# Optimization experiments

Hardware: AMD Instinct MI355X
Metric: run time of the kernel (lower is better)

Reference implementation:

```python
import jax, jax.numpy as jnp
import numpy as np

B, C, N, D, K, M, E, G = 2, 64, 16384, 3, 128, 1, 262144, 3


def setup_inputs() -> dict:
    key = jax.random.key(0)
    ks = jax.random.split(key, 15)
    scale = 1.0 / (C * C)
    return {
        "x": jax.random.normal(ks[0], (B, C, N), jnp.float32),
        "nodes": jax.random.uniform(ks[1], (B, N, D), jnp.float32),
        "node_weights": jax.random.uniform(ks[2], (B, N, M), jnp.float32),
        "geo": jax.random.normal(ks[3], (B, G, N), jnp.float32),
        "directed_edges": jax.random.randint(ks[4], (B, E, 2), 0, N, jnp.int32),
        "edge_gradient_weights": 0.1 * jax.random.normal(ks[5], (B, E, D), jnp.float32),
        "modes": jax.random.normal(ks[6], (K, D, M), jnp.float32),
        "weights_c": scale * jax.random.uniform(ks[7], (C, C, K, M), jnp.float32),
        "weights_s": scale * jax.random.uniform(ks[8], (C, C, K, M), jnp.float32),
        "weights_0": scale * jax.random.uniform(ks[9], (C, C, 1, M), jnp.float32),
        "W": jax.random.normal(ks[10], (C, C), jnp.float32) / np.sqrt(C),
        "gw": jax.random.normal(ks[11], (C, C * D), jnp.float32) / np.sqrt(C * D),
        "geo_wx": jax.random.normal(ks[12], (C, G), jnp.float32) / np.sqrt(G),
        "wx": jax.random.normal(ks[13], (C, C), jnp.float32) / np.sqrt(C),
        "w2": jax.random.normal(ks[14], (C, C), jnp.float32) / np.sqrt(C),
    }


def reference(x, nodes, node_weights, geo, directed_edges, edge_gradient_weights,
              modes, weights_c, weights_s, weights_0, W, gw, geo_wx, wx, w2):
    # ---- Fourier bases: cos(kx), sin(kx), 1 -------------------------------
    temp = jnp.einsum('bxd,kdw->bxkw', nodes, modes)          # [B,N,K,M]
    bases_c, bases_s = jnp.cos(temp), jnp.sin(temp)
    b, n = temp.shape[0], temp.shape[1]
    bases_0 = jnp.ones((b, n, 1, temp.shape[3]), temp.dtype)
    nw = node_weights[:, :, None, :]                          # quadrature weights
    wb_c, wb_s, wb_0 = bases_c * nw, bases_s * nw, bases_0 * nw

    # ---- Spectral convolution (non-uniform Fourier neural layer) ----------
    x_c = jnp.einsum('bix,bxkw->bikw', x, wb_c)
    x_s = -jnp.einsum('bix,bxkw->bikw', x, wb_s)
    x_0 = jnp.einsum('bix,bxkw->bikw', x, wb_0)
    f_c = jnp.einsum('bikw,iokw->bokw', x_c, weights_c) - jnp.einsum('bikw,iokw->bokw', x_s, weights_s)
    f_s = jnp.einsum('bikw,iokw->bokw', x_s, weights_c) + jnp.einsum('bikw,iokw->bokw', x_c, weights_s)
    f_0 = jnp.einsum('bikw,iokw->bokw', x_0, weights_0)
    x1 = (jnp.einsum('bokw,bxkw->box', f_0, bases_0)
          + 2.0 * jnp.einsum('bokw,bxkw->box', f_c, bases_c)
          - 2.0 * jnp.einsum('bokw,bxkw->box', f_s, bases_s))

    # ---- Pointwise linear W ----------------------------------------------
    x2 = jnp.einsum('oi,bix->box', W, x)

    # ---- Least-squares gradient via edge gather + scatter-add -------------
    fT = jnp.transpose(x, (0, 2, 1))                          # [B,N,C]
    tgt, src = directed_edges[..., 0], directed_edges[..., 1]  # [B,E]
    f_src = jnp.take_along_axis(fT, src[:, :, None], axis=1)   # [B,E,C]
    f_tgt = jnp.take_along_axis(fT, tgt[:, :, None], axis=1)
    df = f_src - f_tgt
    # message[b,e,c,d] = w[b,e,d] * df[b,e,c], flattened c-major -> [B,E,C*D]
    msg = (df[..., :, None] * edge_gradient_weights[..., None, :]).reshape(b, tgt.shape[1], -1)
    gradf = jnp.zeros((b, n, msg.shape[-1]), msg.dtype).at[jnp.arange(b)[:, None], tgt].add(msg)
    x3 = jnp.einsum('og,bng->bon', gw, gradf)                  # [B,C,N]

    # ---- Geo embedding: w2 @ (softsign(geo_wx@geo) * (wx@x)) --------------
    h = jax.nn.soft_sign(jnp.einsum('og,bgx->box', geo_wx, geo)) * jnp.einsum('oi,bix->box', wx, x)
    x4 = jnp.einsum('oi,bix->box', w2, h)

    return jax.nn.gelu(x1 + x2 + x3 + x4, approximate=False)
```

## Files before the change

kernel.cpp:

```cpp
#include <hip/hip_runtime.h>
#include <hip/hip_fp16.h>
#include <math.h>

#define BB 2
#define CC 64
#define NN 16384
#define DD 3
#define KK 128
#define EE 262144
#define GG 3
#define PP 128
#define LL (NN/PP)
#define KTOT 576

typedef short bf16x8 __attribute__((ext_vector_type(8)));
typedef float f32x4  __attribute__((ext_vector_type(4)));

__device__ __forceinline__ short f2bf(float f) {
    unsigned u = __float_as_uint(f);
    u += 0x7FFF + ((u >> 16) & 1);
    return (short)(u >> 16);
}
__device__ __forceinline__ float bf2f(unsigned short u) {
    return __uint_as_float(((unsigned)u) << 16);
}

constexpr size_t OFF_XB   = 0;
constexpr size_t OFF_PC   = OFF_XB   + (size_t)BB*NN*32;
constexpr size_t OFF_PS   = OFF_PC   + (size_t)BB*PP*CC*KK;
constexpr size_t OFF_BIN4 = OFF_PC;
constexpr size_t OFF_AC   = OFF_PS   + (size_t)BB*PP*CC*KK;
constexpr size_t OFF_AS   = OFF_AC   + (size_t)BB*CC*KK;
constexpr size_t OFF_F0   = OFF_AS   + (size_t)BB*CC*KK;
constexpr size_t OFF_X0   = OFF_F0   + (size_t)BB*CC;
constexpr size_t OFF_CNT  = OFF_X0   + (size_t)BB*CC;
constexpr size_t OFF_OFFS = OFF_CNT  + (size_t)BB*NN;
constexpr size_t OFF_RANK = OFF_OFFS + (size_t)BB*NN;
constexpr size_t OFF_GRB  = OFF_RANK + (size_t)BB*EE;
constexpr size_t OFF_APAN = OFF_GRB  + (size_t)BB*NN*96;
constexpr size_t OFF_GWXT = OFF_APAN + (size_t)BB*KTOT*CC/2;

__global__ void __launch_bounds__(256) k_pre(const float* __restrict__ x,
                                             const float* __restrict__ nwt,
                                             const int* __restrict__ edges,
                                             const float* __restrict__ W,
                                             const float* __restrict__ gw,
                                             const float* __restrict__ geo_wx,
                                             const float* __restrict__ w2,
                                             unsigned short* __restrict__ xB,
                                             float* __restrict__ x0,
                                             int* __restrict__ counts,
                                             int* __restrict__ rank,
                                             float* __restrict__ gwxT,
                                             short* __restrict__ ApanB) {
    int blk = blockIdx.x;
    int tid = threadIdx.x;
    __shared__ float tile[64][65];
    __shared__ float red[256];
    if (blk < BB*(NN/64)) {
        int b = blk / (NN/64);
        int n0 = (blk % (NN/64)) * 64;
        int c = tid & 63, r4 = tid >> 6;
        for (int rr = 0; rr < 16; rr++) {
            int i = r4*16 + rr;
            tile[i][c] = x[((size_t)b*CC + i)*NN + n0 + c];
        }
        __syncthreads();
        for (int rr = 0; rr < 16; rr++) {
            int nn = r4*16 + rr;
            xB[((size_t)b*NN + n0 + nn)*64 + c] = (unsigned short)f2bf(tile[c][nn]);
        }
    } else if (blk < BB*(NN/64) + BB*CC) {
        int bi = blk - BB*(NN/64);
        int b = bi >> 6, i = bi & 63;
        const float4* __restrict__ xr = (const float4*)&x[((size_t)b*CC + i)*NN];
        const float4* __restrict__ wr = (const float4*)&nwt[(size_t)b*NN];
        float s = 0.f;
        for (int t = tid; t < NN/4; t += 256) {
            float4 xv = xr[t];
            float4 wv = wr[t];
            s += xv.x*wv.x + xv.y*wv.y + xv.z*wv.z + xv.w*wv.w;
        }
        red[tid] = s;
        __syncthreads();
        for (int off = 128; off > 0; off >>= 1) {
            if (tid < off) red[tid] += red[tid+off];
            __syncthreads();
        }
        if (tid == 0) x0[b*CC + i] = red[0];
    } else if (blk < BB*(NN/64) + BB*CC + (BB*EE)/256) {
        int idx = (blk - (BB*(NN/64) + BB*CC))*256 + tid;
        if (idx < BB*EE) {
            int tgt = edges[(size_t)idx*2 + 0];
            int b = idx / EE;
            rank[idx] = atomicAdd(&counts[b*NN + tgt], 1);
        }
    } else {
        int idx = (blk - (BB*(NN/64) + BB*CC + (BB*EE)/256))*256 + tid;
        if (idx < CC*CC) {
            int j = idx>>6, o = idx&63;
            short wv  = f2bf(W[o*CC+j]);
            short w2v = f2bf(w2[o*CC+j]);
            ApanB[((size_t)(0*CC+o))*KTOT + 256 + j] = wv;
            ApanB[((size_t)(1*CC+o))*KTOT + 256 + j] = wv;
            ApanB[((size_t)(0*CC+o))*KTOT + 320 + j] = w2v;
            ApanB[((size_t)(1*CC+o))*KTOT + 320 + j] = w2v;
        }
        if (idx < CC*CC*DD) {
            int g = idx>>6, o = idx&63;
            short gv = f2bf(gw[o*(CC*DD)+g]);
            ApanB[((size_t)(0*CC+o))*KTOT + 384 + g] = gv;
            ApanB[((size_t)(1*CC+o))*KTOT + 384 + g] = gv;
        }
        if (idx < GG*CC) { int g = idx>>6, i = idx&63; gwxT[idx] = geo_wx[i*GG+g]; }
    }
}

__global__ void __launch_bounds__(256) k_a(const float* __restrict__ x,
                                           const float* __restrict__ nwt,
                                           const float* __restrict__ nodes,
                                           const float* __restrict__ modes,
                                           float* __restrict__ pc, float* __restrict__ ps) {
    int bc = blockIdx.x;
    int b = bc / PP, chunk = bc % PP;
    int k0 = blockIdx.y * 64;
    int nbase = chunk * LL;
    int tid = threadIdx.x;
    int lane = tid & 63;
    int w = tid >> 6;
    int col = lane & 15;
    int quad = lane >> 4;

    __shared__ __align__(16) short Axw[64*136];
    __shared__ __align__(16) short Bc [64*136];
    __shared__ __align__(16) short Bsn[64*136];
    __shared__ float ndl[LL*3];

    for (int e = tid; e < LL*3; e += 256) ndl[e] = nodes[((size_t)b*NN + nbase)*3 + e];
#pragma unroll
    for (int s = 0; s < 8; s++) {
        int e = tid + s*256;
        int i = e >> 5, seg = e & 31;
        float4 xv = *(const float4*)&x[((size_t)b*CC + i)*NN + nbase + seg*4];
        float4 wv = *(const float4*)&nwt[(size_t)b*NN + nbase + seg*4];
        unsigned lo = (unsigned)(unsigned short)f2bf(xv.x*wv.x)
                    | ((unsigned)(unsigned short)f2bf(xv.y*wv.y) << 16);
        unsigned hi = (unsigned)(unsigned short)f2bf(xv.z*wv.z)
                    | ((unsigned)(unsigned short)f2bf(xv.w*wv.w) << 16);
        *(uint2*)&Axw[i*136 + seg*4] = make_uint2(lo, hi);
    }
    __syncthreads();
#pragma unroll
    for (int s = 0; s < 32; s++) {
        int e = tid + s*256;
        int n = e & 127, kl = e >> 7;
        int k = k0 + kl;
        float t = ndl[n*3+0]*modes[k*3+0] + ndl[n*3+1]*modes[k*3+1]
                + ndl[n*3+2]*modes[k*3+2];
        Bc [kl*136 + n] = f2bf(__cosf(t));
        Bsn[kl*136 + n] = f2bf(__sinf(t));
    }
    __syncthreads();

    f32x4 ac[4], as4[4];
#pragma unroll
    for (int it = 0; it < 4; it++)
#pragma unroll
        for (int r = 0; r < 4; r++) { ac[it][r] = 0.f; as4[it][r] = 0.f; }

    int rowB = (w*16 + col)*136;
#pragma unroll
    for (int ns = 0; ns < 4; ns++) {
        int koff = ns*32 + quad*8;
        bf16x8 bcf = *(bf16x8*)&Bc [rowB + koff];
        bf16x8 bsf = *(bf16x8*)&Bsn[rowB + koff];
#pragma unroll
        for (int it = 0; it < 4; it++) {
            bf16x8 af = *(bf16x8*)&Axw[(it*16 + col)*136 + koff];
            ac[it]  = __builtin_amdgcn_mfma_f32_16x16x32_bf16(af, bcf, ac[it], 0, 0, 0);
            as4[it] = __builtin_amdgcn_mfma_f32_16x16x32_bf16(af, bsf, as4[it], 0, 0, 0);
        }
    }
    int base = (b*PP + chunk)*CC;
    int kw = k0 + w*16 + col;
#pragma unroll
    for (int it = 0; it < 4; it++) {
#pragma unroll
        for (int r = 0; r < 4; r++) {
            int i = it*16 + quad*4 + r;
            pc[(size_t)(base + i)*KK + kw] = ac[it][r];
            ps[(size_t)(base + i)*KK + kw] = as4[it][r];
        }
    }
}

__global__ void k_ared(const float* __restrict__ pc, const float* __restrict__ ps,
                       float* __restrict__ Ac, float* __restrict__ As) {
    int idx = blockIdx.x*256 + threadIdx.x;
    if (idx >= BB*CC*KK) return;
    int b = idx / (CC*KK);
    int r = idx % (CC*KK);
    float sc = 0.f, ss = 0.f;
    for (int ch = 0; ch < PP; ch++) {
        size_t o = ((size_t)(b*PP + ch)*CC)*KK + r;
        sc += pc[o]; ss += ps[o];
    }
    Ac[idx] = sc; As[idx] = ss;
}

__global__ void __launch_bounds__(256) k_b(const float* __restrict__ Ac, const float* __restrict__ As_,
                                           const float* __restrict__ wc, const float* __restrict__ wsw,
                                           const float* __restrict__ w0, const float* __restrict__ x0,
                                           const int* __restrict__ counts,
                                           int* __restrict__ offsets,
                                           short* __restrict__ ApanB, float* __restrict__ f0) {
    int idx = blockIdx.x;
    int tid = threadIdx.x;
    if (idx >= BB*CC*2) {
        int b = idx - BB*CC*2;
        __shared__ int part[256];
        int base = b*NN + tid*64;
        int s = 0;
        for (int j = 0; j < 64; j++) s += counts[base + j];
        part[tid] = s;
        __syncthreads();
        for (int off = 1; off < 256; off <<= 1) {
            int v = (tid >= off) ? part[tid - off] : 0;
            __syncthreads();
            part[tid] += v;
            __syncthreads();
        }
        int excl = part[tid] - s;
        for (int j = 0; j < 64; j++) {
            int c = counts[base + j];
            offsets[base + j] = excl;
            excl += c;
        }
        return;
    }
    int b = idx / (CC*2);
    int rem = idx % (CC*2);
    int o = rem >> 1, khalf = rem & 1;
    int kl = tid & 63, ig = tid >> 6;
    int k = khalf*64 + kl;
    float fc = 0.f, fs = 0.f;
    for (int ii = 0; ii < 16; ii++) {
        int i = ig*16 + ii;
        float a_c = Ac[(b*CC+i)*KK + k];
        float a_s = As_[(b*CC+i)*KK + k];
        float wcc = wc[((size_t)(i*CC+o))*KK + k];
        float wss = wsw[((size_t)(i*CC+o))*KK + k];
        fc += a_c*wcc + a_s*wss;
        fs += a_c*wss - a_s*wcc;
    }
    __shared__ float rc[256], rs[256];
    __shared__ float f0s[64];
    rc[tid] = fc; rs[tid] = fs;
    if (khalf == 0 && tid < 64) f0s[tid] = x0[b*CC + tid] * w0[tid*CC + o];
    __syncthreads();
    if (ig == 0) {
        fc = rc[kl] + rc[64+kl] + rc[128+kl] + rc[192+kl];
        fs = rs[kl] + rs[64+kl] + rs[128+kl] + rs[192+kl];
        unsigned pk = (unsigned)(unsigned short)f2bf(2.f*fc)
                    | ((unsigned)(unsigned short)f2bf(-2.f*fs) << 16);
        ((unsigned*)ApanB)[((size_t)(b*CC + o))*(KTOT/2) + k] = pk;
    }
    if (khalf == 0 && tid == 0) {
        float acc = 0.f;
        for (int i = 0; i < 64; i++) acc += f0s[i];
        f0[b*CC+o] = acc;
    }
}

__global__ void k_fill(const int* __restrict__ edges, const float* __restrict__ egw,
                       const int* __restrict__ offs, const int* __restrict__ rank,
                       float4* __restrict__ bin4) {
    int idx = blockIdx.x*256 + threadIdx.x;
    if (idx >= BB*EE) return;
    int b = idx / EE;
    int tgt = edges[(size_t)idx*2+0];
    int src = edges[(size_t)idx*2+1];
    const float* __restrict__ ew = &egw[(size_t)idx*3];
    float w0 = ew[0], w1 = ew[1], w2 = ew[2];
    int pos = offs[b*NN+tgt] + rank[idx];
    bin4[(size_t)b*EE + pos] = make_float4(__int_as_float(src), w0, w1, w2);
}

#define ECAP 1024
__global__ void __launch_bounds__(256) k_edge(const unsigned short* __restrict__ xB,
                                              const int* __restrict__ offsets,
                                              const float4* __restrict__ bin4,
                                              unsigned short* __restrict__ gradfB) {
    int blk = blockIdx.x;
    int b = blk / (NN/16);
    int n0 = (blk % (NN/16)) * 16;
    int tid = threadIdx.x;
    int lane = tid & 63;
    int w = tid >> 6;
    __shared__ float4 ebuf[ECAP];
    __shared__ float gl[16][193];
    __shared__ int soff[17];
    if (tid < 16) soff[tid] = offsets[b*NN + n0 + tid];
    if (tid == 16) soff[16] = (n0 + 16 < NN) ? offsets[b*NN + n0 + 16] : EE;
    __syncthreads();
    int base = soff[0];
    int end  = soff[16];
    const unsigned short* __restrict__ xBb = xB + (size_t)b*NN*64 + lane;

    float a0[4], a1[4], a2[4], s0[4], s1[4], s2[4];
#pragma unroll
    for (int q = 0; q < 4; q++) { a0[q]=a1[q]=a2[q]=0.f; s0[q]=s1[q]=s2[q]=0.f; }

    for (int cs = base; cs < end; cs += ECAP) {
        int ce = min(cs + ECAP, end);
        __syncthreads();
        for (int t = cs + tid; t < ce; t += 256)
            ebuf[t - cs] = bin4[(size_t)b*EE + t];
        __syncthreads();
#pragma unroll
        for (int q = 0; q < 4; q++) {
            int nl = w*4 + q;
            int js = max(soff[nl], cs);
            int je = min(soff[nl+1], ce);
#pragma unroll 4
            for (int j = js; j < je; j++) {
                float4 e = ebuf[j - cs];
                int src = __float_as_int(e.x);
                float xs = bf2f(xBb[(size_t)src*64]);
                a0[q] = fmaf(xs, e.y, a0[q]);
                a1[q] = fmaf(xs, e.z, a1[q]);
                a2[q] = fmaf(xs, e.w, a2[q]);
                s0[q] += e.y; s1[q] += e.z; s2[q] += e.w;
            }
        }
    }
    __syncthreads();
#pragma unroll
    for (int q = 0; q < 4; q++) {
        int nl = w*4 + q;
        float xtgt = bf2f(xBb[(size_t)(n0 + nl)*64]);
        gl[nl][lane*3+0] = a0[q] - xtgt*s0[q];
        gl[nl][lane*3+1] = a1[q] - xtgt*s1[q];
        gl[nl][lane*3+2] = a2[q] - xtgt*s2[q];
    }
    __syncthreads();
    for (int t = tid; t < 16*192; t += 256) {
        int nl = t / 192, g = t % 192;
        gradfB[((size_t)(b*NN + n0 + nl))*192 + g] = (unsigned short)f2bf(gl[nl][g]);
    }
}

__global__ void __launch_bounds__(256) k_gemm(const unsigned short* __restrict__ xB,
                                              const float* __restrict__ nodes,
                                              const float* __restrict__ modes,
                                              const float* __restrict__ geo,
                                              const unsigned short* __restrict__ gradfB,
                                              const short* __restrict__ ApanB,
                                              const float* __restrict__ f0,
                                              const float* __restrict__ wx,
                                              const float* __restrict__ gwxT,
                                              float* __restrict__ out) {
    int blk = blockIdx.x;
    int b  = blk >> 8;
    int n0 = (blk & 255) * 64;
    int tid = threadIdx.x;
    int lane = tid & 63;
    int w = tid >> 6;
    int w16 = w * 16;
    int col  = lane & 15;
    int quad = lane >> 4;
    int quad8 = quad * 8;
    int quad4 = quad * 4;

    __shared__ __align__(16) short As[64*72];
    __shared__ __align__(16) short Bs[64*72];
    __shared__ __align__(16) short Ws[64*72];
    __shared__ float ndl[192];
    __shared__ float geo3[192];

    for (int e = tid; e < 4096; e += 256) {
        int i = e >> 6, j = e & 63;
        Ws[i*72 + j] = f2bf(wx[i*64 + j]);
    }
    if (tid < 192) ndl[tid]  = nodes[((size_t)b*NN + n0)*3 + tid];
    if (tid < 192) geo3[tid] = geo[((size_t)b*GG + (tid >> 6))*NN + n0 + (tid & 63)];

    f32x4 acc[4], xwa[4];
    float f0v[4];
#pragma unroll
    for (int r = 0; r < 4; r++) f0v[r] = f0[b*CC + w16 + quad4 + r];
#pragma unroll
    for (int nt = 0; nt < 4; nt++) {
#pragma unroll
        for (int r = 0; r < 4; r++) { acc[nt][r] = f0v[r]; xwa[nt][r] = 0.f; }
    }

    const short* __restrict__ Ab = ApanB + ((size_t)b*CC)*KTOT;

    for (int c = 0; c < 9; c++) {
        __syncthreads();
        for (int e = tid; e < 512; e += 256) {
            int o = e >> 3, seg = e & 7;
            *(uint4*)&As[o*72 + seg*8] =
                *(const uint4*)&Ab[(size_t)o*KTOT + c*64 + seg*8];
        }
        if (c < 4) {
#pragma unroll
            for (int s = 0; s < 8; s++) {
                int e = tid + s*256;
                int n = e >> 5, kpl = e & 31;
                int kp = c*32 + kpl;
                float t = ndl[n*3+0]*modes[kp*3+0] + ndl[n*3+1]*modes[kp*3+1]
                        + ndl[n*3+2]*modes[kp*3+2];
                unsigned pk = (unsigned)(unsigned short)f2bf(__cosf(t))
                            | ((unsigned)(unsigned short)f2bf(__sinf(t)) << 16);
                ((unsigned*)Bs)[n*36 + kpl] = pk;
            }
        } else if (c == 4) {
            for (int e = tid; e < 512; e += 256) {
                int n = e >> 3, seg = e & 7;
                *(uint4*)&Bs[n*72 + seg*8] =
                    *(const uint4*)&xB[((size_t)(b*NN + n0 + n))*64 + seg*8];
            }
        } else if (c == 5) {
#pragma unroll
            for (int r = 0; r < 4; r++) {
                int i = w16 + quad4 + r;
                float g0 = gwxT[i], g1 = gwxT[64+i], g2 = gwxT[128+i];
#pragma unroll
                for (int nt = 0; nt < 4; nt++) {
                    int n = nt*16 + col;
                    float t = g0*geo3[n] + g1*geo3[64+n] + g2*geo3[128+n];
                    float ssv = t / (1.f + fabsf(t));
                    Bs[n*72 + i] = f2bf(ssv * xwa[nt][r]);
                }
            }
        } else {
            const unsigned short* __restrict__ src = gradfB + (size_t)(c-6)*64;
            for (int e = tid; e < 512; e += 256) {
                int n = e >> 3, seg = e & 7;
                *(uint4*)&Bs[n*72 + seg*8] =
                    *(const uint4*)&src[((size_t)(b*NN + n0 + n))*192 + seg*8];
            }
        }
        __syncthreads();
        int rowA = (w16 + col) * 72;
#pragma unroll
        for (int ko = 0; ko < 2; ko++) {
            int koff = ko*32 + quad8;
            bf16x8 af = *(bf16x8*)&As[rowA + koff];
            if (c == 4) {
                bf16x8 wf = *(bf16x8*)&Ws[rowA + koff];
#pragma unroll
                for (int nt = 0; nt < 4; nt++) {
                    bf16x8 bfv = *(bf16x8*)&Bs[(nt*16 + col)*72 + koff];
                    acc[nt] = __builtin_amdgcn_mfma_f32_16x16x32_bf16(af, bfv, acc[nt], 0, 0, 0);
                    xwa[nt] = __builtin_amdgcn_mfma_f32_16x16x32_bf16(wf, bfv, xwa[nt], 0, 0, 0);
                }
            } else {
#pragma unroll
                for (int nt = 0; nt < 4; nt++) {
                    bf16x8 bfv = *(bf16x8*)&Bs[(nt*16 + col)*72 + koff];
                    acc[nt] = __builtin_amdgcn_mfma_f32_16x16x32_bf16(af, bfv, acc[nt], 0, 0, 0);
                }
            }
        }
    }
#pragma unroll
    for (int nt = 0; nt < 4; nt++) {
#pragma unroll
        for (int r = 0; r < 4; r++) {
            int o = w16 + quad4 + r;
            float v = acc[nt][r];
            float g = 0.5f * v * (1.f + erff(v * 0.70710678118654752f));
            out[((size_t)b*CC + o)*NN + n0 + nt*16 + col] = g;
        }
    }
}

extern "C" void kernel_launch(void* const* d_in, const int* in_sizes, int n_in,
                              void* d_out, int out_size, void* d_ws, size_t ws_size,
                              hipStream_t stream) {
    const float* x      = (const float*)d_in[0];
    const float* nodes  = (const float*)d_in[1];
    const float* nwt    = (const float*)d_in[2];
    const float* geo    = (const float*)d_in[3];
    const int*   edges  = (const int*)d_in[4];
    const float* egw    = (const float*)d_in[5];
    const float* modes  = (const float*)d_in[6];
    const float* wc     = (const float*)d_in[7];
    const float* wsw    = (const float*)d_in[8];
    const float* w0     = (const float*)d_in[9];
    const float* W      = (const float*)d_in[10];
    const float* gw     = (const float*)d_in[11];
    const float* geo_wx = (const float*)d_in[12];
    const float* wx     = (const float*)d_in[13];
    const float* w2     = (const float*)d_in[14];

    float* ws   = (float*)d_ws;
    unsigned short* xB  = (unsigned short*)(ws + OFF_XB);
    float* pc   = ws + OFF_PC;
    float* ps   = ws + OFF_PS;
    float* Ac   = ws + OFF_AC;
    float* As_  = ws + OFF_AS;
    float* f0   = ws + OFF_F0;
    float* x0   = ws + OFF_X0;
    int*  counts = (int*)(ws + OFF_CNT);
    int*  offs   = (int*)(ws + OFF_OFFS);
    int*  rank   = (int*)(ws + OFF_RANK);
    float4* bin4 = (float4*)(ws + OFF_BIN4);
    unsigned short* gradfB = (unsigned short*)(ws + OFF_GRB);
    short* ApanB  = (short*)(ws + OFF_APAN);
    float* gwxT   = ws + OFF_GWXT;
    float* out  = (float*)d_out;

    hipMemsetAsync(counts, 0, (size_t)(BB*NN)*sizeof(int), stream);

    int npre = BB*(NN/64) + BB*CC + (BB*EE)/256 + 48;
    k_pre  <<<npre, 256, 0, stream>>>(x, nwt, edges, W, gw, geo_wx, w2,
                                      xB, x0, counts, rank, gwxT, ApanB);
    k_a    <<<dim3(BB*PP, 2), 256, 0, stream>>>(x, nwt, nodes, modes, pc, ps);
    k_ared <<<(BB*CC*KK)/256, 256, 0, stream>>>(pc, ps, Ac, As_);
    k_b    <<<BB*CC*2 + BB, 256, 0, stream>>>(Ac, As_, wc, wsw, w0, x0, counts, offs, ApanB, f0);
    k_fill <<<(BB*EE)/256, 256, 0, stream>>>(edges, egw, offs, rank, bin4);
    k_edge <<<BB*(NN/16), 256, 0, stream>>>(xB, offs, bin4, gradfB);
    k_gemm <<<BB*(NN/64), 256, 0, stream>>>(xB, nodes, modes, geo, gradfB, ApanB, f0,
                                            wx, gwxT, out);
}
```

Measured before the change: 212.8 us.

## Fuse preprocessing, spectral projection, reduction and edge-binning into fewer launches

Merges k_pre with the spectral projection kernel k_a into one heterogeneous launch, merges the partial-sum reduction with the count prefix scan, and merges the spectral weight mix with the edge-bin fill. Kernel launches drop from seven to five, and independent work now shares a grid. The spectral projection tile is halved to 32 modes per block, giving more blocks and less shared memory per block. The reduction uses four lanes per output with shuffles. The cost is a larger shared-memory footprint for every block in the fused kernel and mixed branch work inside one grid.

Measured after the change: 198.3 us. 1.07x faster.

```diff
diff --git a/kernel.cpp b/kernel.cpp
--- a/kernel.cpp
+++ b/kernel.cpp
@@ -40,24 +40,33 @@
 constexpr size_t OFF_APAN = OFF_GRB  + (size_t)BB*NN*96;
 constexpr size_t OFF_GWXT = OFF_APAN + (size_t)BB*KTOT*CC/2;
 
-__global__ void __launch_bounds__(256) k_pre(const float* __restrict__ x,
-                                             const float* __restrict__ nwt,
-                                             const int* __restrict__ edges,
-                                             const float* __restrict__ W,
-                                             const float* __restrict__ gw,
-                                             const float* __restrict__ geo_wx,
-                                             const float* __restrict__ w2,
-                                             unsigned short* __restrict__ xB,
-                                             float* __restrict__ x0,
-                                             int* __restrict__ counts,
-                                             int* __restrict__ rank,
-                                             float* __restrict__ gwxT,
-                                             short* __restrict__ ApanB) {
+#define S_A0 (BB*(NN/64))
+#define S_A1 (S_A0 + BB*CC)
+#define S_A2 (S_A1 + (BB*EE)/256)
+#define S_A3 (S_A2 + 48)
+#define S_A4 (S_A3 + BB*PP*4)
+__global__ void __launch_bounds__(256) k1(const float* __restrict__ x,
+                                          const float* __restrict__ nwt,
+                                          const int* __restrict__ edges,
+                                          const float* __restrict__ W,
+                                          const float* __restrict__ gw,
+                                          const float* __restrict__ geo_wx,
+                                          const float* __restrict__ w2,
+                                          const float* __restrict__ nodes,
+                                          const float* __restrict__ modes,
+                                          unsigned short* __restrict__ xB,
+                                          float* __restrict__ x0,
+                                          int* __restrict__ counts,
+                                          int* __restrict__ rank,
+                                          float* __restrict__ gwxT,
+                                          short* __restrict__ ApanB,
+                                          float* __restrict__ pc,
+                                          float* __restrict__ ps) {
     int blk = blockIdx.x;
     int tid = threadIdx.x;
-    __shared__ float tile[64][65];
-    __shared__ float red[256];
-    if (blk < BB*(NN/64)) {
+    __shared__ __align__(16) char smem[36864];
+    if (blk < S_A0) {
+        float (*tile)[65] = (float (*)[65])smem;
         int b = blk / (NN/64);
         int n0 = (blk % (NN/64)) * 64;
         int c = tid & 63, r4 = tid >> 6;
@@ -70,8 +79,9 @@
             int nn = r4*16 + rr;
             xB[((size_t)b*NN + n0 + nn)*64 + c] = (unsigned short)f2bf(tile[c][nn]);
         }
-    } else if (blk < BB*(NN/64) + BB*CC) {
-        int bi = blk - BB*(NN/64);
+    } else if (blk < S_A1) {
+        float* red = (float*)smem;
+        int bi = blk - S_A0;
         int b = bi >> 6, i = bi & 63;
         const float4* __restrict__ xr = (const float4*)&x[((size_t)b*CC + i)*NN];
         const float4* __restrict__ wr = (const float4*)&nwt[(size_t)b*NN];
@@ -88,15 +98,13 @@
             __syncthreads();
         }
         if (tid == 0) x0[b*CC + i] = red[0];
-    } else if (blk < BB*(NN/64) + BB*CC + (BB*EE)/256) {
-        int idx = (blk - (BB*(NN/64) + BB*CC))*256 + tid;
-        if (idx < BB*EE) {
-            int tgt = edges[(size_t)idx*2 + 0];
-            int b = idx / EE;
-            rank[idx] = atomicAdd(&counts[b*NN + tgt], 1);
-        }
-    } else {
-        int idx = (blk - (BB*(NN/64) + BB*CC + (BB*EE)/256))*256 + tid;
+    } else if (blk < S_A2) {
+        int idx = (blk - S_A1)*256 + tid;
+        int tgt = edges[(size_t)idx*2 + 0];
+        int b = idx / EE;
+        rank[idx] = atomicAdd(&counts[b*NN + tgt], 1);
+    } else if (blk < S_A3) {
+        int idx = (blk - S_A2)*256 + tid;
         if (idx < CC*CC) {
             int j = idx>>6, o = idx&63;
             short wv  = f2bf(W[o*CC+j]);
@@ -113,111 +121,107 @@
             ApanB[((size_t)(1*CC+o))*KTOT + 384 + g] = gv;
         }
         if (idx < GG*CC) { int g = idx>>6, i = idx&63; gwxT[idx] = geo_wx[i*GG+g]; }
-    }
-}
-
-__global__ void __launch_bounds__(256) k_a(const float* __restrict__ x,
-                                           const float* __restrict__ nwt,
-                                           const float* __restrict__ nodes,
-                                           const float* __restrict__ modes,
-                                           float* __restrict__ pc, float* __restrict__ ps) {
-    int bc = blockIdx.x;
-    int b = bc / PP, chunk = bc % PP;
-    int k0 = blockIdx.y * 64;
-    int nbase = chunk * LL;
+    } else {
+        short* Axw = (short*)smem;
+        short* Bc  = (short*)(smem + 17408);
+        short* Bsn = (short*)(smem + 17408 + 8704);
+        float* ndl = (float*)(smem + 17408 + 8704 + 8704);
+        int bc = blk - S_A3;
+        int b = bc >> 9;
+        int rem = bc & 511;
+        int chunk = rem >> 2;
+        int kt = rem & 3;
+        int k0 = kt * 32;
+        int nbase = chunk * LL;
+        int lane = tid & 63;
+        int w = tid >> 6;
+        int col = lane & 15;
+        int quad = lane >> 4;
+        int wk = w & 1;
+        int wi = w >> 1;
+
+        for (int e = tid; e < LL*3; e += 256) ndl[e] = nodes[((size_t)b*NN + nbase)*3 + e];
+#pragma unroll
+        for (int s = 0; s < 8; s++) {
+            int e = tid + s*256;
+            int i = e >> 5, seg = e & 31;
+            float4 xv = *(const float4*)&x[((size_t)b*CC + i)*NN + nbase + seg*4];
+            float4 wv = *(const float4*)&nwt[(size_t)b*NN + nbase + seg*4];
+            unsigned lo = (unsigned)(unsigned short)f2bf(xv.x*wv.x)
+                        | ((unsigned)(unsigned short)f2bf(xv.y*wv.y) << 16);
+            unsigned hi = (unsigned)(unsigned short)f2bf(xv.z*wv.z)
+                        | ((unsigned)(unsigned short)f2bf(xv.w*wv.w) << 16);
+            *(uint2*)&Axw[i*136 + seg*4] = make_uint2(lo, hi);
+        }
+        __syncthreads();
+#pragma unroll
+        for (int s = 0; s < 16; s++) {
+            int e = tid + s*256;
+            int n = e & 127, kl = e >> 7;
+            int k = k0 + kl;
+            float t = ndl[n*3+0]*modes[k*3+0] + ndl[n*3+1]*modes[k*3+1]
+                    + ndl[n*3+2]*modes[k*3+2];
+            Bc [kl*136 + n] = f2bf(__cosf(t));
+            Bsn[kl*136 + n] = f2bf(__sinf(t));
+        }
+        __syncthreads();
+
+        f32x4 ac[2], as4[2];
+#pragma unroll
+        for (int it = 0; it < 2; it++)
+#pragma unroll
+            for (int r = 0; r < 4; r++) { ac[it][r] = 0.f; as4[it][r] = 0.f; }
+
+        int rowB = (wk*16 + col)*136;
+#pragma unroll
+        for (int ns = 0; ns < 4; ns++) {
+            int koff = ns*32 + quad*8;
+            bf16x8 bcf = *(bf16x8*)&Bc [rowB + koff];
+            bf16x8 bsf = *(bf16x8*)&Bsn[rowB + koff];
+#pragma unroll
+            for (int it = 0; it < 2; it++) {
+                int itile = wi*2 + it;
+                bf16x8 af = *(bf16x8*)&Axw[(itile*16 + col)*136 + koff];
+                ac[it]  = __builtin_amdgcn_mfma_f32_16x16x32_bf16(af, bcf, ac[it], 0, 0, 0);
+                as4[it] = __builtin_amdgcn_mfma_f32_16x16x32_bf16(af, bsf, as4[it], 0, 0, 0);
+            }
+        }
+        int base = (b*PP + chunk)*CC;
+        int kw = k0 + wk*16 + col;
+#pragma unroll
+        for (int it = 0; it < 2; it++) {
+#pragma unroll
+            for (int r = 0; r < 4; r++) {
+                int i = (wi*2 + it)*16 + quad*4 + r;
+                pc[(size_t)(base + i)*KK + kw] = ac[it][r];
+                ps[(size_t)(base + i)*KK + kw] = as4[it][r];
+            }
+        }
+    }
+}
+
+__global__ void __launch_bounds__(256) k2(const float* __restrict__ pc, const float* __restrict__ ps,
+                                          float* __restrict__ Ac, float* __restrict__ As,
+                                          const int* __restrict__ counts,
+                                          int* __restrict__ offsets) {
+    int blk = blockIdx.x;
     int tid = threadIdx.x;
-    int lane = tid & 63;
-    int w = tid >> 6;
-    int col = lane & 15;
-    int quad = lane >> 4;
-
-    __shared__ __align__(16) short Axw[64*136];
-    __shared__ __align__(16) short Bc [64*136];
-    __shared__ __align__(16) short Bsn[64*136];
-    __shared__ float ndl[LL*3];
-
-    for (int e = tid; e < LL*3; e += 256) ndl[e] = nodes[((size_t)b*NN + nbase)*3 + e];
-#pragma unroll
-    for (int s = 0; s < 8; s++) {
-        int e = tid + s*256;
-        int i = e >> 5, seg = e & 31;
-        float4 xv = *(const float4*)&x[((size_t)b*CC + i)*NN + nbase + seg*4];
-        float4 wv = *(const float4*)&nwt[(size_t)b*NN + nbase + seg*4];
-        unsigned lo = (unsigned)(unsigned short)f2bf(xv.x*wv.x)
-                    | ((unsigned)(unsigned short)f2bf(xv.y*wv.y) << 16);
-        unsigned hi = (unsigned)(unsigned short)f2bf(xv.z*wv.z)
-                    | ((unsigned)(unsigned short)f2bf(xv.w*wv.w) << 16);
-        *(uint2*)&Axw[i*136 + seg*4] = make_uint2(lo, hi);
-    }
-    __syncthreads();
-#pragma unroll
-    for (int s = 0; s < 32; s++) {
-        int e = tid + s*256;
-        int n = e & 127, kl = e >> 7;
-        int k = k0 + kl;
-        float t = ndl[n*3+0]*modes[k*3+0] + ndl[n*3+1]*modes[k*3+1]
-                + ndl[n*3+2]*modes[k*3+2];
-        Bc [kl*136 + n] = f2bf(__cosf(t));
-        Bsn[kl*136 + n] = f2bf(__sinf(t));
-    }
-    __syncthreads();
-
-    f32x4 ac[4], as4[4];
-#pragma unroll
-    for (int it = 0; it < 4; it++)
-#pragma unroll
-        for (int r = 0; r < 4; r++) { ac[it][r] = 0.f; as4[it][r] = 0.f; }
-
-    int rowB = (w*16 + col)*136;
-#pragma unroll
-    for (int ns = 0; ns < 4; ns++) {
-        int koff = ns*32 + quad*8;
-        bf16x8 bcf = *(bf16x8*)&Bc [rowB + koff];
-        bf16x8 bsf = *(bf16x8*)&Bsn[rowB + koff];
-#pragma unroll
-        for (int it = 0; it < 4; it++) {
-            bf16x8 af = *(bf16x8*)&Axw[(it*16 + col)*136 + koff];
-            ac[it]  = __builtin_amdgcn_mfma_f32_16x16x32_bf16(af, bcf, ac[it], 0, 0, 0);
-            as4[it] = __builtin_amdgcn_mfma_f32_16x16x32_bf16(af, bsf, as4[it], 0, 0, 0);
-        }
-    }
-    int base = (b*PP + chunk)*CC;
-    int kw = k0 + w*16 + col;
-#pragma unroll
-    for (int it = 0; it < 4; it++) {
-#pragma unroll
-        for (int r = 0; r < 4; r++) {
-            int i = it*16 + quad*4 + r;
-            pc[(size_t)(base + i)*KK + kw] = ac[it][r];
-            ps[(size_t)(base + i)*KK + kw] = as4[it][r];
-        }
-    }
-}
-
-__global__ void k_ared(const float* __restrict__ pc, const float* __restrict__ ps,
-                       float* __restrict__ Ac, float* __restrict__ As) {
-    int idx = blockIdx.x*256 + threadIdx.x;
-    if (idx >= BB*CC*KK) return;
-    int b = idx / (CC*KK);
-    int r = idx % (CC*KK);
-    float sc = 0.f, ss = 0.f;
-    for (int ch = 0; ch < PP; ch++) {
-        size_t o = ((size_t)(b*PP + ch)*CC)*KK + r;
-        sc += pc[o]; ss += ps[o];
-    }
-    Ac[idx] = sc; As[idx] = ss;
-}
-
-__global__ void __launch_bounds__(256) k_b(const float* __restrict__ Ac, const float* __restrict__ As_,
-                                           const float* __restrict__ wc, const float* __restrict__ wsw,
-                                           const float* __restrict__ w0, const float* __restrict__ x0,
-                                           const int* __restrict__ counts,
-                                           int* __restrict__ offsets,
-                                           short* __restrict__ ApanB, float* __restrict__ f0) {
-    int idx = blockIdx.x;
-    int tid = threadIdx.x;
-    if (idx >= BB*CC*2) {
-        int b = idx - BB*CC*2;
+    if (blk < 256) {
+        int idx = blk*64 + (tid >> 2);
+        int sub = tid & 3;
+        if (idx >= BB*CC*KK) return;
+        int b = idx / (CC*KK);
+        int r = idx % (CC*KK);
+        float sc = 0.f, ss = 0.f;
+        for (int ch = sub; ch < PP; ch += 4) {
+            size_t o = ((size_t)(b*PP + ch)*CC)*KK + r;
+            sc += pc[o]; ss += ps[o];
+        }
+        sc += __shfl_xor(sc, 1); sc += __shfl_xor(sc, 2);
+        ss += __shfl_xor(ss, 1); ss += __shfl_xor(ss, 2);
+        if (sub == 0) { Ac[idx] = sc; As[idx] = ss; }
+    } else {
+        int b = blk - 256;
         __shared__ int part[256];
         int base = b*NN + tid*64;
         int s = 0;
@@ -236,6 +240,27 @@
             offsets[base + j] = excl;
             excl += c;
         }
+    }
+}
+
+__global__ void __launch_bounds__(256) k3(const float* __restrict__ Ac, const float* __restrict__ As_,
+                                          const float* __restrict__ wc, const float* __restrict__ wsw,
+                                          const float* __restrict__ w0, const float* __restrict__ x0,
+                                          const int* __restrict__ edges, const float* __restrict__ egw,
+                                          const int* __restrict__ offs, const int* __restrict__ rank,
+                                          float4* __restrict__ bin4,
+                                          short* __restrict__ ApanB, float* __restrict__ f0) {
+    int idx = blockIdx.x;
+    int tid = threadIdx.x;
+    if (idx >= BB*CC*2) {
+        int e = (idx - BB*CC*2)*256 + tid;
+        int b = e / EE;
+        int tgt = edges[(size_t)e*2+0];
+        int src = edges[(size_t)e*2+1];
+        const float* __restrict__ ew = &egw[(size_t)e*3];
+        float e0 = ew[0], e1 = ew[1], e2 = ew[2];
+        int pos = offs[b*NN+tgt] + rank[e];
+        bin4[(size_t)b*EE + pos] = make_float4(__int_as_float(src), e0, e1, e2);
         return;
     }
     int b = idx / (CC*2);
@@ -270,20 +295,6 @@
         for (int i = 0; i < 64; i++) acc += f0s[i];
         f0[b*CC+o] = acc;
     }
-}
-
-__global__ void k_fill(const int* __restrict__ edges, const float* __restrict__ egw,
-                       const int* __restrict__ offs, const int* __restrict__ rank,
-                       float4* __restrict__ bin4) {
-    int idx = blockIdx.x*256 + threadIdx.x;
-    if (idx >= BB*EE) return;
-    int b = idx / EE;
-    int tgt = edges[(size_t)idx*2+0];
-    int src = edges[(size_t)idx*2+1];
-    const float* __restrict__ ew = &egw[(size_t)idx*3];
-    float w0 = ew[0], w1 = ew[1], w2 = ew[2];
-    int pos = offs[b*NN+tgt] + rank[idx];
-    bin4[(size_t)b*EE + pos] = make_float4(__int_as_float(src), w0, w1, w2);
 }
 
 #define ECAP 1024
@@ -516,13 +527,11 @@
 
     hipMemsetAsync(counts, 0, (size_t)(BB*NN)*sizeof(int), stream);
 
-    int npre = BB*(NN/64) + BB*CC + (BB*EE)/256 + 48;
-    k_pre  <<<npre, 256, 0, stream>>>(x, nwt, edges, W, gw, geo_wx, w2,
-                                      xB, x0, counts, rank, gwxT, ApanB);
-    k_a    <<<dim3(BB*PP, 2), 256, 0, stream>>>(x, nwt, nodes, modes, pc, ps);
-    k_ared <<<(BB*CC*KK)/256, 256, 0, stream>>>(pc, ps, Ac, As_);
-    k_b    <<<BB*CC*2 + BB, 256, 0, stream>>>(Ac, As_, wc, wsw, w0, x0, counts, offs, ApanB, f0);
-    k_fill <<<(BB*EE)/256, 256, 0, stream>>>(edges, egw, offs, rank, bin4);
+    k1 <<<S_A4, 256, 0, stream>>>(x, nwt, edges, W, gw, geo_wx, w2, nodes, modes,
+                                  xB, x0, counts, rank, gwxT, ApanB, pc, ps);
+    k2 <<<256 + BB, 256, 0, stream>>>(pc, ps, Ac, As_, counts, offs);
+    k3 <<<BB*CC*2 + (BB*EE)/256, 256, 0, stream>>>(Ac, As_, wc, wsw, w0, x0,
+                                                   edges, egw, offs, rank, bin4, ApanB, f0);
     k_edge <<<BB*(NN/16), 256, 0, stream>>>(xB, offs, bin4, gradfB);
     k_gemm <<<BB*(NN/64), 256, 0, stream>>>(xB, nodes, modes, geo, gradfB, ApanB, f0,
                                             wx, gwxT, out);
```
